# Kernel optimization log

Measured on AMD Instinct MI355X. Metric: run time of the kernel, lower is better.

Reference implementation:

```python
import jax, jax.numpy as jnp
import numpy as np

B, CIN, H, W = 4, 64, 128, 128
COUT, K, S, P = 64, 3, 1, 1


def setup_inputs() -> dict:
    key = jax.random.key(0)
    k1, k2, k3, k4 = jax.random.split(key, 4)
    x = jax.random.normal(k1, (B, CIN, H, W), jnp.float32)
    # offset-predicting conv params (small scale so offsets stay in a sane range)
    offset_w = jax.random.normal(k2, (2 * K * K, CIN, K, K), jnp.float32) * 0.01
    offset_b = jnp.zeros((2 * K * K,), jnp.float32)
    # deformable conv params
    fan_in = CIN * K * K
    deform_w = jax.random.normal(k3, (COUT, CIN, K, K), jnp.float32) / np.sqrt(fan_in).astype(np.float32)
    deform_b = jax.random.normal(k4, (COUT,), jnp.float32) * 0.01
    return {"x": x, "offset_w": offset_w, "offset_b": offset_b,
            "deform_w": deform_w, "deform_b": deform_b}


def _conv2d(x, w, b, stride, pad):
    y = jax.lax.conv_general_dilated(
        x, w, window_strides=(stride, stride),
        padding=[(pad, pad), (pad, pad)],
        dimension_numbers=("NCHW", "OIHW", "NCHW"))
    return y + b[None, :, None, None]


def _deform_conv2d(x, offset, w, b, stride, pad):
    Bn, C, Hi, Wi = x.shape
    O, _, Kh, Kw = w.shape
    KK = Kh * Kw
    Ho = (Hi + 2 * pad - Kh) // stride + 1
    Wo = (Wi + 2 * pad - Kw) // stride + 1
    # offset layout (torchvision/mmcv): [B, KK, 2, Ho, Wo] with (dy, dx)
    off = offset.reshape(Bn, KK, 2, Ho, Wo)
    dy, dx = off[:, :, 0], off[:, :, 1]
    ky, kx = jnp.meshgrid(jnp.arange(Kh), jnp.arange(Kw), indexing="ij")
    ky = ky.reshape(-1).astype(x.dtype)  # [KK]
    kx = kx.reshape(-1).astype(x.dtype)
    hgrid = (jnp.arange(Ho) * stride - pad).astype(x.dtype)  # [Ho]
    wgrid = (jnp.arange(Wo) * stride - pad).astype(x.dtype)  # [Wo]
    # fractional sampling coords [B, KK, Ho, Wo]
    ys = hgrid[None, None, :, None] + ky[None, :, None, None] + dy
    xs = wgrid[None, None, None, :] + kx[None, :, None, None] + dx
    y0 = jnp.floor(ys)
    x0 = jnp.floor(xs)
    ly = (ys - y0)[:, None]  # [B,1,KK,Ho,Wo] for channel broadcast
    lx = (xs - x0)[:, None]
    y0i = y0.astype(jnp.int32)
    x0i = x0.astype(jnp.int32)

    def samp(yi, xi):
        valid = (yi >= 0) & (yi < Hi) & (xi >= 0) & (xi < Wi)
        yc = jnp.clip(yi, 0, Hi - 1)
        xc = jnp.clip(xi, 0, Wi - 1)
        # per-batch gather -> [B, C, KK, Ho, Wo]
        v = jax.vmap(lambda im, yy, xx: im[:, yy, xx])(x, yc, xc)
        return v * valid[:, None].astype(x.dtype)

    v00 = samp(y0i, x0i)
    v01 = samp(y0i, x0i + 1)
    v10 = samp(y0i + 1, x0i)
    v11 = samp(y0i + 1, x0i + 1)
    sampled = (v00 * (1 - ly) * (1 - lx) + v01 * (1 - ly) * lx
               + v10 * ly * (1 - lx) + v11 * ly * lx)  # [B,C,KK,Ho,Wo]
    out = jnp.einsum("bckhw,ock->bohw", sampled, w.reshape(O, C, KK))
    return out + b[None, :, None, None]


def reference(x, offset_w, offset_b, deform_w, deform_b):
    offset = _conv2d(x, offset_w, offset_b, S, P)
    return _deform_conv2d(x, offset, deform_w, deform_b, S, P)
```

## Files before the change

kernel.cpp:

```cpp
#include <hip/hip_runtime.h>
#include <hip/hip_bf16.h>

#define B_    4
#define CIN_  64
#define H_    128
#define W_    128
#define COUT_ 64
#define KK_   9
#define OFFC_ 18
#define HW_   (H_*W_)
#define TILE_ 64

typedef short bf8  __attribute__((ext_vector_type(8)));
typedef float f32x4 __attribute__((ext_vector_type(4)));

__device__ inline short f2bf(float f) {
    union { __hip_bfloat16 h; short s; } u; u.h = __float2bfloat16(f); return u.s;
}
__device__ inline float bf2f(short s) {
    union { unsigned u; float f; } v; v.u = ((unsigned)(unsigned short)s) << 16; return v.f;
}

__global__ __launch_bounds__(256) void prep_all(
    const float* __restrict__ x,
    const float* __restrict__ ow, const float* __restrict__ dw,
    short* __restrict__ xt, short* __restrict__ dwbf, short* __restrict__ owbf)
{
    const int tid = threadIdx.x;
    const int bid = blockIdx.x;
    if (bid < 1024) {
        const int b  = bid >> 8;
        const int pb = bid & 255;
        const int p  = tid & 63;
        const int g  = tid >> 6;
        const int pix = pb * 64 + p;
        const float* src = x + ((size_t)b * CIN_ + g * 16) * HW_ + pix;
        short vals[16];
        #pragma unroll
        for (int j = 0; j < 16; ++j) vals[j] = f2bf(src[(size_t)j * HW_]);
        short* dst = xt + ((size_t)b * HW_ + pix) * 64 + g * 16;
        *(bf8*)dst       = *(bf8*)&vals[0];
        *(bf8*)(dst + 8) = *(bf8*)&vals[8];
    } else {
        const int idx = (bid - 1024) * 256 + tid;
        {
            const int k = idx / (COUT_ * CIN_);
            const int r = idx % (COUT_ * CIN_);
            const int o = r >> 6, c = r & 63;
            dwbf[idx] = f2bf(dw[(o * CIN_ + c) * KK_ + k]);
        }
        if (idx < KK_ * 32 * CIN_) {
            const int k = idx / (32 * CIN_);
            const int r = idx % (32 * CIN_);
            const int co = r >> 6, c = r & 63;
            owbf[idx] = f2bf(co < OFFC_ ? ow[(co * CIN_ + c) * KK_ + k] : 0.0f);
        }
    }
}

#define DECL_SET(S) \
    bf8 r00a##S, r00b##S, r01a##S, r01b##S, r10a##S, r10b##S, r11a##S, r11b##S; \
    float pm0##S, pm1##S, pm2##S, pm3##S;

#define LOAD_SET(S, t) { \
    const int ky = (t) / 3, kx = (t) % 3; \
    const float dy = offs[(2 * (t) + 0) * TILE_ + p]; \
    const float dx = offs[(2 * (t) + 1) * TILE_ + p]; \
    const float ys = (float)(ho + ky - 1) + dy; \
    const float xs = (float)(wo + kx - 1) + dx; \
    const float y0f = floorf(ys), x0f = floorf(xs); \
    const float ly = ys - y0f, lx = xs - x0f; \
    const int y0 = (int)y0f, x0 = (int)x0f; \
    const int y1 = y0 + 1,   x1 = x0 + 1; \
    const bool y0v = (y0 >= 0) & (y0 < H_); \
    const bool y1v = (y1 >= 0) & (y1 < H_); \
    const bool x0v = (x0 >= 0) & (x0 < W_); \
    const bool x1v = (x1 >= 0) & (x1 < W_); \
    pm0##S = (y0v & x0v) ? (1.f - ly) * (1.f - lx) : 0.f; \
    pm1##S = (y0v & x1v) ? (1.f - ly) * lx         : 0.f; \
    pm2##S = (y1v & x0v) ? ly * (1.f - lx)         : 0.f; \
    pm3##S = (y1v & x1v) ? ly * lx                 : 0.f; \
    const int y0c = min(max(y0, 0), H_ - 1); \
    const int y1c = min(max(y1, 0), H_ - 1); \
    const int x0c = min(max(x0, 0), W_ - 1); \
    const int x1c = min(max(x1, 0), W_ - 1); \
    const short* c00 = xbt + (size_t)(y0c * W_ + x0c) * 64 + sub * 8; \
    const short* c01 = xbt + (size_t)(y0c * W_ + x1c) * 64 + sub * 8; \
    const short* c10 = xbt + (size_t)(y1c * W_ + x0c) * 64 + sub * 8; \
    const short* c11 = xbt + (size_t)(y1c * W_ + x1c) * 64 + sub * 8; \
    r00a##S = *(const bf8*)(c00); r00b##S = *(const bf8*)(c00 + 32); \
    r01a##S = *(const bf8*)(c01); r01b##S = *(const bf8*)(c01 + 32); \
    r10a##S = *(const bf8*)(c10); r10b##S = *(const bf8*)(c10 + 32); \
    r11a##S = *(const bf8*)(c11); r11b##S = *(const bf8*)(c11 + 32); \
}

#define COMBINE_WRITE(S, dstbuf) { \
    bf8 va, vb; \
    _Pragma("unroll") \
    for (int j = 0; j < 8; ++j) { \
        const float sa = pm0##S * bf2f(r00a##S[j]) + pm1##S * bf2f(r01a##S[j]) \
                       + pm2##S * bf2f(r10a##S[j]) + pm3##S * bf2f(r11a##S[j]); \
        const float sb = pm0##S * bf2f(r00b##S[j]) + pm1##S * bf2f(r01b##S[j]) \
                       + pm2##S * bf2f(r10b##S[j]) + pm3##S * bf2f(r11b##S[j]); \
        va[j] = f2bf(sa); \
        vb[j] = f2bf(sb); \
    } \
    const int cA = sub; \
    const int cB = sub + 4; \
    *(bf8*)&u.smp[(dstbuf) * 4096 + p * 64 + ((cA ^ (p & 7)) << 3)] = va; \
    *(bf8*)&u.smp[(dstbuf) * 4096 + p * 64 + ((cB ^ (p & 7)) << 3)] = vb; \
}

__global__ __launch_bounds__(256, 4) void fused_deform_mfma(
    const short* __restrict__ xt,
    const short* __restrict__ owbf,
    const float* __restrict__ obias,
    const short* __restrict__ dwbf,
    const float* __restrict__ dbias,
    float* __restrict__ out)
{
    __shared__ union {
        short xtl[3 * 66 * 64];
        short smp[4 * 64 * 64];
    } u;
    __shared__ float offs[OFFC_ * TILE_];

    const int lin  = blockIdx.x;
    const int nid  = (lin & 7) * 128 + (lin >> 3);
    const int b    = nid >> 8;
    const int tile = nid & 255;

    const int tid = threadIdx.x;
    const int pixbase = tile * TILE_;
    const int ho    = pixbase >> 7;
    const int wbase = pixbase & (W_ - 1);
    const int lane  = tid & 63;
    const int wv    = tid >> 6;
    const int arow  = lane & 15;
    const int kseg  = lane >> 4;

    const short* xbt = xt + (size_t)b * HW_ * 64;

    for (int base = 0; base < 3 * 66 * 8; base += 256) {
        const int idx = base + tid;
        if (idx < 3 * 66 * 8) {
            const int cc = idx & 7;
            const int qy = idx >> 3;
            const int y  = qy / 66;
            const int q  = qy - y * 66;
            const int gy = ho + y - 1;
            const int gx = wbase + q - 1;
            bf8 v;
            if (gy >= 0 && gy < H_ && gx >= 0 && gx < W_) {
                v = *(const bf8*)&xbt[(size_t)(gy * W_ + gx) * 64 + cc * 8];
            } else {
                #pragma unroll
                for (int j = 0; j < 8; ++j) v[j] = 0;
            }
            *(bf8*)&u.xtl[(y * 66 + q) * 64 + ((cc ^ (q & 7)) << 3)] = v;
        }
    }
    __syncthreads();

    {
        const int m = wv & 1;
        const int h = wv >> 1;
        f32x4 acca[2];
        acca[0] = (f32x4)0.f; acca[1] = (f32x4)0.f;
        for (int t = 0; t < KK_; ++t) {
            const int ky = t / 3, kx = t % 3;
            #pragma unroll
            for (int kc = 0; kc < 2; ++kc) {
                const int cbase = kc * 32 + kseg * 8;
                const bf8 afrag = *(const bf8*)&owbf[(t * 32 + m * 16 + arow) * 64 + cbase];
                const int cchunk = cbase >> 3;
                #pragma unroll
                for (int nt = 0; nt < 2; ++nt) {
                    const int pp = h * 32 + nt * 16 + arow;
                    const int q = pp + kx;
                    const bf8 bfrag = *(const bf8*)&u.xtl[(ky * 66 + q) * 64 + ((cchunk ^ (q & 7)) << 3)];
                    acca[nt] = __builtin_amdgcn_mfma_f32_16x16x32_bf16(afrag, bfrag, acca[nt], 0, 0, 0);
                }
            }
        }
        #pragma unroll
        for (int nt = 0; nt < 2; ++nt) {
            #pragma unroll
            for (int r = 0; r < 4; ++r) {
                const int co = m * 16 + kseg * 4 + r;
                if (co < OFFC_) {
                    const int pp = h * 32 + nt * 16 + arow;
                    offs[co * TILE_ + pp] = acca[nt][r] + obias[co];
                }
            }
        }
    }
    __syncthreads();

    const int pix16 = lane >> 2;
    const int sub   = lane & 3;
    const int p     = wv * 16 + pix16;
    const int wo    = wbase + p;

    DECL_SET(A)
    DECL_SET(B)

    f32x4 accb[4];
    #pragma unroll
    for (int nt = 0; nt < 4; ++nt) accb[nt] = (f32x4)0.f;

    auto mfmaTap = [&](int t, int srcbuf) {
        #pragma unroll
        for (int kc = 0; kc < 2; ++kc) {
            const int cbase = kc * 32 + kseg * 8;
            const bf8 afrag = *(const bf8*)&dwbf[(t * 64 + wv * 16 + arow) * 64 + cbase];
            const int cchunk = cbase >> 3;
            #pragma unroll
            for (int nt = 0; nt < 4; ++nt) {
                const int pp = nt * 16 + arow;
                const bf8 bfrag = *(const bf8*)&u.smp[srcbuf * 4096 + pp * 64 + ((cchunk ^ (pp & 7)) << 3)];
                accb[nt] = __builtin_amdgcn_mfma_f32_16x16x32_bf16(afrag, bfrag, accb[nt], 0, 0, 0);
            }
        }
    };

    LOAD_SET(A, 0)
    LOAD_SET(B, 1)
    COMBINE_WRITE(A, 0)
    COMBINE_WRITE(B, 1)
    __syncthreads();

    #pragma unroll
    for (int r = 0; r < 4; ++r) {
        const int ta = 2 * r + 2;
        const int tb = 2 * r + 3;
        const int sb = ((r + 1) & 1) * 2;
        const int cb = (r & 1) * 2;
        LOAD_SET(A, ta)
        if (tb < KK_) LOAD_SET(B, tb)
        mfmaTap(2 * r,     cb + 0);
        mfmaTap(2 * r + 1, cb + 1);
        COMBINE_WRITE(A, sb + 0)
        if (tb < KK_) COMBINE_WRITE(B, sb + 1)
        __syncthreads();
    }
    mfmaTap(8, 0);

    float* ob = out + (size_t)b * COUT_ * HW_ + pixbase;
    #pragma unroll
    for (int nt = 0; nt < 4; ++nt) {
        const int pp = nt * 16 + arow;
        #pragma unroll
        for (int r = 0; r < 4; ++r) {
            const int o = wv * 16 + kseg * 4 + r;
            ob[(size_t)o * HW_ + pp] = accb[nt][r] + dbias[o];
        }
    }
}

extern "C" void kernel_launch(void* const* d_in, const int* in_sizes, int n_in,
                              void* d_out, int out_size, void* d_ws, size_t ws_size,
                              hipStream_t stream) {
    const float* x        = (const float*)d_in[0];
    const float* offset_w = (const float*)d_in[1];
    const float* offset_b = (const float*)d_in[2];
    const float* deform_w = (const float*)d_in[3];
    const float* deform_b = (const float*)d_in[4];
    float* out = (float*)d_out;

    short* dwbf = (short*)d_ws;
    short* owbf = (short*)((char*)d_ws + 73728);
    short* xt   = (short*)((char*)d_ws + 110592);

    prep_all<<<1024 + 144, 256, 0, stream>>>(x, offset_w, deform_w, xt, dwbf, owbf);

    fused_deform_mfma<<<1024, 256, 0, stream>>>(xt, owbf, offset_b, dwbf, deform_b, out);
}
```

Baseline: 46.68 us.

## Halve pixel tile to 32 with 128-thread blocks and remap MFMA work

Shrinks the per-block pixel tile from 64 to 32 and the block from 256 to 128 threads, doubling the grid to 2048 blocks. The halo tile, sample buffers and offset buffer shrink to match. Each wave now covers 32 output channels by 32 pixels in the deform GEMM and 16 offset channels in the offset conv. The aim is more blocks in flight, less LDS per block and better occupancy. In exchange the halo overhead per pixel grows (34 columns per 32 pixels instead of 66 per 64) and weight fragments are reloaded across twice as many blocks.

New measurement: 53.71 us. 1.15x slower.

```diff
diff --git a/kernel.cpp b/kernel.cpp
--- a/kernel.cpp
+++ b/kernel.cpp
@@ -9,7 +9,9 @@
 #define KK_   9
 #define OFFC_ 18
 #define HW_   (H_*W_)
-#define TILE_ 64
+#define TILE_ 32
+#define PW_   34
+#define SMPSZ (TILE_*64)
 
 typedef short bf8  __attribute__((ext_vector_type(8)));
 typedef float f32x4 __attribute__((ext_vector_type(4)));
@@ -107,11 +109,11 @@
     } \
     const int cA = sub; \
     const int cB = sub + 4; \
-    *(bf8*)&u.smp[(dstbuf) * 4096 + p * 64 + ((cA ^ (p & 7)) << 3)] = va; \
-    *(bf8*)&u.smp[(dstbuf) * 4096 + p * 64 + ((cB ^ (p & 7)) << 3)] = vb; \
-}
-
-__global__ __launch_bounds__(256, 4) void fused_deform_mfma(
+    *(bf8*)&u.smp[(dstbuf) * SMPSZ + p * 64 + ((cA ^ (p & 7)) << 3)] = va; \
+    *(bf8*)&u.smp[(dstbuf) * SMPSZ + p * 64 + ((cB ^ (p & 7)) << 3)] = vb; \
+}
+
+__global__ __launch_bounds__(128, 4) void fused_deform_mfma(
     const short* __restrict__ xt,
     const short* __restrict__ owbf,
     const float* __restrict__ obias,
@@ -120,15 +122,15 @@
     float* __restrict__ out)
 {
     __shared__ union {
-        short xtl[3 * 66 * 64];
-        short smp[4 * 64 * 64];
+        short xtl[3 * PW_ * 64];
+        short smp[4 * SMPSZ];
     } u;
     __shared__ float offs[OFFC_ * TILE_];
 
     const int lin  = blockIdx.x;
-    const int nid  = (lin & 7) * 128 + (lin >> 3);
-    const int b    = nid >> 8;
-    const int tile = nid & 255;
+    const int nid  = (lin & 7) * 256 + (lin >> 3);
+    const int b    = nid >> 9;
+    const int tile = nid & 511;
 
     const int tid = threadIdx.x;
     const int pixbase = tile * TILE_;
@@ -141,13 +143,13 @@
 
     const short* xbt = xt + (size_t)b * HW_ * 64;
 
-    for (int base = 0; base < 3 * 66 * 8; base += 256) {
+    for (int base = 0; base < 3 * PW_ * 8; base += 128) {
         const int idx = base + tid;
-        if (idx < 3 * 66 * 8) {
+        if (idx < 3 * PW_ * 8) {
             const int cc = idx & 7;
             const int qy = idx >> 3;
-            const int y  = qy / 66;
-            const int q  = qy - y * 66;
+            const int y  = qy / PW_;
+            const int q  = qy - y * PW_;
             const int gy = ho + y - 1;
             const int gx = wbase + q - 1;
             bf8 v;
@@ -157,14 +159,12 @@
                 #pragma unroll
                 for (int j = 0; j < 8; ++j) v[j] = 0;
             }
-            *(bf8*)&u.xtl[(y * 66 + q) * 64 + ((cc ^ (q & 7)) << 3)] = v;
+            *(bf8*)&u.xtl[(y * PW_ + q) * 64 + ((cc ^ (q & 7)) << 3)] = v;
         }
     }
     __syncthreads();
 
     {
-        const int m = wv & 1;
-        const int h = wv >> 1;
         f32x4 acca[2];
         acca[0] = (f32x4)0.f; acca[1] = (f32x4)0.f;
         for (int t = 0; t < KK_; ++t) {
@@ -172,13 +172,13 @@
             #pragma unroll
             for (int kc = 0; kc < 2; ++kc) {
                 const int cbase = kc * 32 + kseg * 8;
-                const bf8 afrag = *(const bf8*)&owbf[(t * 32 + m * 16 + arow) * 64 + cbase];
+                const bf8 afrag = *(const bf8*)&owbf[(t * 32 + wv * 16 + arow) * 64 + cbase];
                 const int cchunk = cbase >> 3;
                 #pragma unroll
                 for (int nt = 0; nt < 2; ++nt) {
-                    const int pp = h * 32 + nt * 16 + arow;
+                    const int pp = nt * 16 + arow;
                     const int q = pp + kx;
-                    const bf8 bfrag = *(const bf8*)&u.xtl[(ky * 66 + q) * 64 + ((cchunk ^ (q & 7)) << 3)];
+                    const bf8 bfrag = *(const bf8*)&u.xtl[(ky * PW_ + q) * 64 + ((cchunk ^ (q & 7)) << 3)];
                     acca[nt] = __builtin_amdgcn_mfma_f32_16x16x32_bf16(afrag, bfrag, acca[nt], 0, 0, 0);
                 }
             }
@@ -187,9 +187,9 @@
         for (int nt = 0; nt < 2; ++nt) {
             #pragma unroll
             for (int r = 0; r < 4; ++r) {
-                const int co = m * 16 + kseg * 4 + r;
+                const int co = wv * 16 + kseg * 4 + r;
                 if (co < OFFC_) {
-                    const int pp = h * 32 + nt * 16 + arow;
+                    const int pp = nt * 16 + arow;
                     offs[co * TILE_ + pp] = acca[nt][r] + obias[co];
                 }
             }
@@ -197,29 +197,32 @@
     }
     __syncthreads();
 
-    const int pix16 = lane >> 2;
-    const int sub   = lane & 3;
-    const int p     = wv * 16 + pix16;
-    const int wo    = wbase + p;
+    const int p   = tid >> 2;
+    const int sub = tid & 3;
+    const int wo  = wbase + p;
 
     DECL_SET(A)
     DECL_SET(B)
 
     f32x4 accb[4];
     #pragma unroll
-    for (int nt = 0; nt < 4; ++nt) accb[nt] = (f32x4)0.f;
+    for (int i = 0; i < 4; ++i) accb[i] = (f32x4)0.f;
 
     auto mfmaTap = [&](int t, int srcbuf) {
         #pragma unroll
-        for (int kc = 0; kc < 2; ++kc) {
-            const int cbase = kc * 32 + kseg * 8;
-            const bf8 afrag = *(const bf8*)&dwbf[(t * 64 + wv * 16 + arow) * 64 + cbase];
-            const int cchunk = cbase >> 3;
-            #pragma unroll
-            for (int nt = 0; nt < 4; ++nt) {
-                const int pp = nt * 16 + arow;
-                const bf8 bfrag = *(const bf8*)&u.smp[srcbuf * 4096 + pp * 64 + ((cchunk ^ (pp & 7)) << 3)];
-                accb[nt] = __builtin_amdgcn_mfma_f32_16x16x32_bf16(afrag, bfrag, accb[nt], 0, 0, 0);
+        for (int mm = 0; mm < 2; ++mm) {
+            const int m = wv * 2 + mm;
+            #pragma unroll
+            for (int kc = 0; kc < 2; ++kc) {
+                const int cbase = kc * 32 + kseg * 8;
+                const bf8 afrag = *(const bf8*)&dwbf[(t * 64 + m * 16 + arow) * 64 + cbase];
+                const int cchunk = cbase >> 3;
+                #pragma unroll
+                for (int nt = 0; nt < 2; ++nt) {
+                    const int pp = nt * 16 + arow;
+                    const bf8 bfrag = *(const bf8*)&u.smp[srcbuf * SMPSZ + pp * 64 + ((cchunk ^ (pp & 7)) << 3)];
+                    accb[mm * 2 + nt] = __builtin_amdgcn_mfma_f32_16x16x32_bf16(afrag, bfrag, accb[mm * 2 + nt], 0, 0, 0);
+                }
             }
         }
     };
@@ -248,12 +251,15 @@
 
     float* ob = out + (size_t)b * COUT_ * HW_ + pixbase;
     #pragma unroll
-    for (int nt = 0; nt < 4; ++nt) {
-        const int pp = nt * 16 + arow;
-        #pragma unroll
-        for (int r = 0; r < 4; ++r) {
-            const int o = wv * 16 + kseg * 4 + r;
-            ob[(size_t)o * HW_ + pp] = accb[nt][r] + dbias[o];
+    for (int mm = 0; mm < 2; ++mm) {
+        #pragma unroll
+        for (int nt = 0; nt < 2; ++nt) {
+            const int pp = nt * 16 + arow;
+            #pragma unroll
+            for (int r = 0; r < 4; ++r) {
+                const int o = wv * 32 + mm * 16 + kseg * 4 + r;
+                ob[(size_t)o * HW_ + pp] = accb[mm * 2 + nt][r] + dbias[o];
+            }
         }
     }
 }
@@ -274,5 +280,5 @@
 
     prep_all<<<1024 + 144, 256, 0, stream>>>(x, offset_w, deform_w, xt, dwbf, owbf);
 
-    fused_deform_mfma<<<1024, 256, 0, stream>>>(xt, owbf, offset_b, dwbf, deform_b, out);
-}
+    fused_deform_mfma<<<2048, 128, 0, stream>>>(xt, owbf, offset_b, dwbf, deform_b, out);
+}
```
